# Performance work log

Measured on AMD Instinct MI355X. Metric: run time of the kernel, lower is better.

The kernel has to match this reference:

```python
import math
import jax, jax.numpy as jnp
import numpy as np

B, S, E = 8, 4096, 512


def setup_inputs() -> dict:
    key = jax.random.key(0)
    ks = jax.random.split(key, 8)
    w = 0.02
    return {
        "state1": jax.random.normal(ks[0], (B, S, E), jnp.float32),
        "state2": jax.random.normal(ks[1], (B, S, E), jnp.float32),
        "Wq": jax.random.normal(ks[2], (E, E), jnp.float32) * w,
        "bq": jax.random.normal(ks[3], (E,), jnp.float32) * w,
        "Wk": jax.random.normal(ks[4], (E, E), jnp.float32) * w,
        "bk": jax.random.normal(ks[5], (E,), jnp.float32) * w,
        "Wv": jax.random.normal(ks[6], (E, E), jnp.float32) * w,
        "bv": jax.random.normal(ks[7], (E,), jnp.float32) * w,
    }


def reference(state1, state2, Wq, bq, Wk, bk, Wv, bv):
    b, s, e = state1.shape
    num_blocks = max(1, int(math.ceil(s ** (2.0 / 3.0))))  # 256 for S=4096
    block_size = int(math.ceil(s / num_blocks))            # 16; exact tiling
    scale = math.sqrt(e)

    def proj(x, W, bias):  # torch Linear: x @ W.T + b
        return x @ W.T + bias

    # fold blocks into a batch dimension: [B, nb, bs, E]
    x1 = state1.reshape(b, num_blocks, block_size, e)
    x2 = state2.reshape(b, num_blocks, block_size, e)

    q1, k1, v1 = proj(x1, Wq, bq), proj(x1, Wk, bk), proj(x1, Wv, bv)
    q2, k2, v2 = proj(x2, Wq, bq), proj(x2, Wk, bk), proj(x2, Wv, bv)

    # block-diagonal bidirectional cross attention (dropout = eval/no-op)
    attn12 = jax.nn.softmax(jnp.einsum('bnqe,bnke->bnqk', q1, k2) / scale, axis=-1)
    out1 = jnp.einsum('bnqk,bnke->bnqe', attn12, v2).reshape(b, s, e)

    attn21 = jax.nn.softmax(jnp.einsum('bnqe,bnke->bnqk', q2, k1) / scale, axis=-1)
    out2 = jnp.einsum('bnqk,bnke->bnqe', attn21, v1).reshape(b, s, e)

    return out1, out2
```

## Files before the change

kernel.cpp:

```cpp
#include <hip/hip_runtime.h>
#include <hip/hip_bf16.h>

typedef __attribute__((ext_vector_type(4))) float f32x4;
typedef __attribute__((ext_vector_type(8))) short short8;
typedef __attribute__((ext_vector_type(4))) short short4v;

#define EDIM 512
#define WELEMS 262144

static __device__ __forceinline__ short f2bf(float f) {
  union { float f; unsigned u; } v; v.f = f;
  unsigned r = v.u + 0x7fffu + ((v.u >> 16) & 1u);
  return (short)(r >> 16);
}
static __device__ __forceinline__ float bf2f(short s) {
  union { float f; unsigned u; } v; v.u = ((unsigned)(unsigned short)s) << 16;
  return v.f;
}

static __device__ __forceinline__ void gload_lds16(const short* g, short* l) {
  __builtin_amdgcn_global_load_lds(
      (const __attribute__((address_space(1))) unsigned int*)g,
      (__attribute__((address_space(3))) unsigned int*)(unsigned int)(unsigned long long)l,
      16, 0, 0);
}

__global__ __launch_bounds__(256) void prep(
    const float* __restrict__ Wq, const float* __restrict__ bq,
    const float* __restrict__ Wk, const float* __restrict__ Wv,
    short* __restrict__ Wvb, float* __restrict__ tvec, short* __restrict__ Hb) {
  __shared__ float sh[2][64][33];
  const int b = blockIdx.x;
  const int tid = threadIdx.x;
  if (b < 256) {
    int i = (b * 256 + tid) * 4;
    f32x4 v = *(const f32x4*)(Wv + i);
    short4v vs;
#pragma unroll
    for (int j = 0; j < 4; ++j) vs[j] = f2bf(v[j]);
    *(short4v*)(Wvb + i) = vs;
  } else if (b < 264) {
    float* red = &sh[0][0][0];
    const int fl = tid & 63;
    const int part = tid >> 6;
    const int f = (b - 256) * 64 + fl;
    float s = 0.f;
    const int n0 = part * 128;
#pragma unroll 8
    for (int n = n0; n < n0 + 128; ++n) s += Wk[(size_t)n * EDIM + f] * bq[n];
    red[part * 64 + fl] = s;
    __syncthreads();
    if (part == 0)
      tvec[f] = ((red[fl] + red[64 + fl]) + (red[128 + fl] + red[192 + fl]));
  } else {
    const int hb = b - 264;
    const int bf = (hb >> 4) * 32;
    const int be = (hb & 15) * 32;
    const int fh = (tid & 15) * 2;
    const int eh = (tid >> 4) * 2;
    float a00 = 0, a01 = 0, a10 = 0, a11 = 0;
    for (int nc = 0; nc < 8; ++nc) {
      __syncthreads();
#pragma unroll
      for (int p = 0; p < 8; ++p) {
        const int idx = p * 256 + tid;
        const int n = idx >> 5, f = idx & 31;
        sh[0][n][f] = Wk[(size_t)(nc * 64 + n) * EDIM + bf + f];
        sh[1][n][f] = Wq[(size_t)(nc * 64 + n) * EDIM + be + f];
      }
      __syncthreads();
#pragma unroll 4
      for (int n = 0; n < 64; ++n) {
        const float k0 = sh[0][n][fh], k1 = sh[0][n][fh + 1];
        const float q0 = sh[1][n][eh], q1 = sh[1][n][eh + 1];
        a00 += k0 * q0; a01 += k0 * q1; a10 += k1 * q0; a11 += k1 * q1;
      }
    }
    Hb[(size_t)(bf + fh) * EDIM + be + eh] = f2bf(a00);
    Hb[(size_t)(bf + fh) * EDIM + be + eh + 1] = f2bf(a01);
    Hb[(size_t)(bf + fh + 1) * EDIM + be + eh] = f2bf(a10);
    Hb[(size_t)(bf + fh + 1) * EDIM + be + eh + 1] = f2bf(a11);
  }
}

__global__ __launch_bounds__(256) void convert_x(
    const float* __restrict__ s1, const float* __restrict__ s2,
    const float* __restrict__ tvec,
    short* __restrict__ o1, short* __restrict__ o2,
    float* __restrict__ w1, float* __restrict__ w2) {
  const int wv = threadIdx.x >> 6, lane = threadIdx.x & 63;
  const size_t r = (size_t)blockIdx.x * 4 + wv;
  const int off = lane * 8;
  const f32x4 t0 = *(const f32x4*)(tvec + off);
  const f32x4 t1 = *(const f32x4*)(tvec + off + 4);
#pragma unroll
  for (int st = 0; st < 2; ++st) {
    const float* src = st ? s2 : s1;
    f32x4 a0 = *(const f32x4*)(src + r * EDIM + off);
    f32x4 a1 = *(const f32x4*)(src + r * EDIM + off + 4);
    short8 rb;
    float dot = 0.f;
#pragma unroll
    for (int j = 0; j < 4; ++j) {
      rb[j] = f2bf(a0[j]); dot += a0[j] * t0[j];
      rb[j + 4] = f2bf(a1[j]); dot += a1[j] * t1[j];
    }
    *(short8*)((st ? o2 : o1) + r * EDIM + off) = rb;
#pragma unroll
    for (int d = 1; d < 64; d <<= 1) dot += __shfl_xor(dot, d);
    if (lane == 0) (st ? w2 : w1)[r] = dot;
  }
}

__global__ __launch_bounds__(256, 3) void proj_t(
    const short* __restrict__ S1b, const short* __restrict__ S2b,
    const short* __restrict__ Hb,
    short* __restrict__ TV, size_t McE, int mblocks) {
  __shared__ short Al[128 * 64];
  __shared__ short Bl[128 * 64];

  int mb, zn;
  {
    const int L = blockIdx.x;
    if ((mblocks & 7) == 0) {
      const int mpx = mblocks >> 3;
      const int xcd = L & 7;
      const int slot = L >> 3;
      mb = xcd * mpx + slot / 8;
      zn = slot % 8;
    } else { mb = L / 8; zn = L % 8; }
  }
  const int z = zn >> 2;
  const int nb = zn & 3;

  const short* __restrict__ X = z ? S2b : S1b;
  short* __restrict__ O = TV + (size_t)z * McE;

  const int m0 = mb * 128;
  const int n0 = nb * 128;
  const int tid = threadIdx.x;
  const int lane = tid & 63;
  const int wv = tid >> 6;
  const int wr = wv >> 1, wc = wv & 1;
  const int col = lane & 15;
  const int kg = lane >> 4;

  f32x4 acc[4][4] = {};

  for (int ks = 0; ks < EDIM / 64; ++ks) {
    const int k0 = ks * 64;
    __syncthreads();
#pragma unroll
    for (int j = 0; j < 4; ++j) {
      const int g = (j * 4 + wv) * 64 + lane;
      const int row = g >> 3;
      const int sc = (g & 7) ^ (row & 7);
      gload_lds16(X + (size_t)(m0 + row) * EDIM + k0 + sc * 8, Al + (j * 4 + wv) * 512);
      gload_lds16(Hb + (size_t)(n0 + row) * EDIM + k0 + sc * 8, Bl + (j * 4 + wv) * 512);
    }
    __syncthreads();
#pragma unroll
    for (int kk = 0; kk < 2; ++kk) {
      short8 af[4], bf8[4];
#pragma unroll
      for (int i = 0; i < 4; ++i) {
        const int ra = wr * 64 + i * 16 + col;
        const int rb = wc * 64 + i * 16 + col;
        af[i]  = *(const short8*)(Al + ra * 64 + ((((kk << 2) + kg) ^ (ra & 7)) << 3));
        bf8[i] = *(const short8*)(Bl + rb * 64 + ((((kk << 2) + kg) ^ (rb & 7)) << 3));
      }
#pragma unroll
      for (int mi = 0; mi < 4; ++mi)
#pragma unroll
        for (int nj = 0; nj < 4; ++nj)
          acc[mi][nj] = __builtin_amdgcn_mfma_f32_16x16x32_bf16(af[mi], bf8[nj], acc[mi][nj], 0, 0, 0);
    }
  }

#pragma unroll
  for (int mi = 0; mi < 4; ++mi) {
#pragma unroll
    for (int j = 0; j < 4; ++j) {
      const size_t r = m0 + wr * 64 + mi * 16 + kg * 4 + j;
#pragma unroll
      for (int nj = 0; nj < 4; ++nj) {
        const int e = n0 + wc * 64 + nj * 16 + col;
        O[r * EDIM + e] = f2bf(acc[mi][nj][j]);
      }
    }
  }
}

__global__ __launch_bounds__(256) void attn_y(
    const short* __restrict__ TV, const short* __restrict__ S1b, const short* __restrict__ S2b,
    const float* __restrict__ w1, const float* __restrict__ w2, size_t McE) {
  __shared__ float plds[4][16][16];
  const int dir = blockIdx.y;
  const short* __restrict__ Q = TV + (size_t)dir * McE;
  const short* __restrict__ KV = dir ? S1b : S2b;
  const float* __restrict__ w = dir ? w1 : w2;
  short* __restrict__ Y = (short*)TV + (size_t)(2 + dir) * McE;

  const int lane = threadIdx.x & 63;
  const int wv = threadIdx.x >> 6;
  const size_t r0 = ((size_t)blockIdx.x * 4 + wv) * 16;
  const int col = lane & 15;
  const int kg = lane >> 4;

  const short* Qp = Q + (r0 + col) * EDIM + kg * 8;
  const short* Kp = KV + (r0 + col) * EDIM + kg * 8;
  f32x4 s = {};
#pragma unroll
  for (int ks = 0; ks < 16; ++ks) {
    short8 a = *(const short8*)(Qp + ks * 32);
    short8 b = *(const short8*)(Kp + ks * 32);
    s = __builtin_amdgcn_mfma_f32_16x16x32_bf16(a, b, s, 0, 0, 0);
  }
  const float scale = 0.04419417382415922f;
  const float wj = w[r0 + col];
  float p[4];
#pragma unroll
  for (int j = 0; j < 4; ++j) p[j] = (s[j] + wj) * scale;
#pragma unroll
  for (int j = 0; j < 4; ++j) {
    float m = p[j];
#pragma unroll
    for (int d = 1; d < 16; d <<= 1) m = fmaxf(m, __shfl_xor(m, d));
    float e = __expf(p[j] - m);
    float ssum = e;
#pragma unroll
    for (int d = 1; d < 16; d <<= 1) ssum += __shfl_xor(ssum, d);
    p[j] = e / ssum;
  }
#pragma unroll
  for (int j = 0; j < 4; ++j) plds[wv][kg * 4 + j][col] = p[j];
  __syncthreads();

  const int e0 = lane * 8;
  short8 v8[16];
#pragma unroll
  for (int k = 0; k < 16; ++k) v8[k] = *(const short8*)(KV + (r0 + k) * EDIM + e0);
#pragma unroll
  for (int q = 0; q < 16; ++q) {
    float acc[8] = {0, 0, 0, 0, 0, 0, 0, 0};
#pragma unroll
    for (int k = 0; k < 16; ++k) {
      const float pv = plds[wv][q][k];
#pragma unroll
      for (int i = 0; i < 8; ++i) acc[i] += pv * bf2f(v8[k][i]);
    }
    short8 y;
#pragma unroll
    for (int i = 0; i < 8; ++i) y[i] = f2bf(acc[i]);
    *(short8*)(Y + (r0 + q) * EDIM + e0) = y;
  }
}

__global__ __launch_bounds__(256, 3) void out_gemm(
    const short* __restrict__ TV, const short* __restrict__ Wvb,
    const float* __restrict__ bv,
    float* __restrict__ out1, float* __restrict__ out2, size_t McE, int mblocks) {
  __shared__ short Al[128 * 64];
  __shared__ short Bl[128 * 64];

  int mb, zn;
  {
    const int L = blockIdx.x;
    if ((mblocks & 7) == 0) {
      const int mpx = mblocks >> 3;
      const int xcd = L & 7;
      const int slot = L >> 3;
      mb = xcd * mpx + slot / 8;
      zn = slot % 8;
    } else { mb = L / 8; zn = L % 8; }
  }
  const int z = zn >> 2;
  const int nb = zn & 3;

  const short* __restrict__ A = TV + (size_t)(2 + z) * McE;
  float* __restrict__ O = z ? out2 : out1;

  const int m0 = mb * 128;
  const int n0 = nb * 128;
  const int tid = threadIdx.x;
  const int lane = tid & 63;
  const int wv = tid >> 6;
  const int wr = wv >> 1, wc = wv & 1;
  const int col = lane & 15;
  const int kg = lane >> 4;

  f32x4 acc[4][4] = {};

  for (int ks = 0; ks < EDIM / 64; ++ks) {
    const int k0 = ks * 64;
    __syncthreads();
#pragma unroll
    for (int j = 0; j < 4; ++j) {
      const int g = (j * 4 + wv) * 64 + lane;
      const int row = g >> 3;
      const int sc = (g & 7) ^ (row & 7);
      gload_lds16(A + (size_t)(m0 + row) * EDIM + k0 + sc * 8, Al + (j * 4 + wv) * 512);
      gload_lds16(Wvb + (size_t)(n0 + row) * EDIM + k0 + sc * 8, Bl + (j * 4 + wv) * 512);
    }
    __syncthreads();
#pragma unroll
    for (int kk = 0; kk < 2; ++kk) {
      short8 af[4], bf8[4];
#pragma unroll
      for (int i = 0; i < 4; ++i) {
        const int ra = wr * 64 + i * 16 + col;
        const int rb = wc * 64 + i * 16 + col;
        af[i]  = *(const short8*)(Al + ra * 64 + ((((kk << 2) + kg) ^ (ra & 7)) << 3));
        bf8[i] = *(const short8*)(Bl + rb * 64 + ((((kk << 2) + kg) ^ (rb & 7)) << 3));
      }
#pragma unroll
      for (int mi = 0; mi < 4; ++mi)
#pragma unroll
        for (int nj = 0; nj < 4; ++nj)
          acc[mi][nj] = __builtin_amdgcn_mfma_f32_16x16x32_bf16(af[mi], bf8[nj], acc[mi][nj], 0, 0, 0);
    }
  }

#pragma unroll
  for (int mi = 0; mi < 4; ++mi) {
#pragma unroll
    for (int j = 0; j < 4; ++j) {
      const size_t r = m0 + wr * 64 + mi * 16 + kg * 4 + j;
#pragma unroll
      for (int nj = 0; nj < 4; ++nj) {
        const int e = n0 + wc * 64 + nj * 16 + col;
        O[r * EDIM + e] = acc[mi][nj][j] + bv[e];
      }
    }
  }
}

extern "C" void kernel_launch(void* const* d_in, const int* in_sizes, int n_in,
                              void* d_out, int out_size, void* d_ws, size_t ws_size,
                              hipStream_t stream) {
  const float* state1 = (const float*)d_in[0];
  const float* state2 = (const float*)d_in[1];
  const float* Wq = (const float*)d_in[2];
  const float* bq = (const float*)d_in[3];
  const float* Wk = (const float*)d_in[4];
  const float* Wv = (const float*)d_in[6];
  const float* bv = (const float*)d_in[7];

  const size_t Mtot = (size_t)8 * 4096;
  float* out1 = (float*)d_out;
  float* out2 = out1 + Mtot * EDIM;

  short* Wvb = (short*)d_ws;
  short* Hb = Wvb + WELEMS;
  float* tvec = (float*)(Hb + WELEMS);
  float* w1 = tvec + EDIM;
  float* w2 = w1 + Mtot;
  short* base = (short*)(w2 + Mtot);

  const size_t fixed_bytes = (size_t)(2 * WELEMS) * 2 + (EDIM + 2 * Mtot) * 4;
  size_t nch = 1;
  while (nch < 256) {
    size_t need = fixed_bytes + (size_t)6 * (Mtot / nch) * EDIM * 2;
    if (need <= ws_size) break;
    nch <<= 1;
  }
  const size_t Mc = Mtot / nch;
  const size_t McE = Mc * EDIM;
  const int mblocks = (int)(Mc / 128);
  short* S1b = base;
  short* S2b = S1b + McE;
  short* TV = S2b + McE;

  prep<<<dim3(520), dim3(256), 0, stream>>>(Wq, bq, Wk, Wv, Wvb, tvec, Hb);

  for (size_t c = 0; c < nch; ++c) {
    const size_t roff = c * Mc;
    convert_x<<<dim3((unsigned)(Mc / 4)), dim3(256), 0, stream>>>(
        state1 + roff * EDIM, state2 + roff * EDIM, tvec, S1b, S2b, w1 + roff, w2 + roff);
    proj_t<<<dim3((unsigned)(mblocks * 8)), dim3(256), 0, stream>>>(
        S1b, S2b, Hb, TV, McE, mblocks);
    attn_y<<<dim3((unsigned)(Mc / 64), 2), dim3(256), 0, stream>>>(
        TV, S1b, S2b, w1 + roff, w2 + roff, McE);
    out_gemm<<<dim3((unsigned)(mblocks * 8)), dim3(256), 0, stream>>>(
        TV, Wvb, bv, out1 + roff * EDIM, out2 + roff * EDIM, McE, mblocks);
  }
}
```

Before: 200.1 us.

## Merge weight prep into conversion kernel and compute key-bias term inside attention

The separate prep kernel is folded into the per-chunk conversion launch, so weight preprocessing runs as extra blocks of the first chunk's conversion grid. The per-row dot product of the keys with tvec moves out of the conversion kernel into attn_y, where it is computed from the bf16 keys already loaded for the score MFMA. This drops one launch and the w1/w2 workspace arrays. It adds ALU work in attn_y and now uses bf16-rounded keys for the bias term. The conversion blocks in the merged launch do not read tvec, so the new grid does not race on it.

```diff
diff --git a/kernel.cpp b/kernel.cpp
--- a/kernel.cpp
+++ b/kernel.cpp
@@ -25,90 +25,80 @@
       16, 0, 0);
 }
 
-__global__ __launch_bounds__(256) void prep(
+__global__ __launch_bounds__(256) void prep_convert(
+    const float* __restrict__ s1, const float* __restrict__ s2,
     const float* __restrict__ Wq, const float* __restrict__ bq,
     const float* __restrict__ Wk, const float* __restrict__ Wv,
-    short* __restrict__ Wvb, float* __restrict__ tvec, short* __restrict__ Hb) {
+    short* __restrict__ Wvb, float* __restrict__ tvec, short* __restrict__ Hb,
+    short* __restrict__ o1, short* __restrict__ o2, int prep_blocks) {
   __shared__ float sh[2][64][33];
   const int b = blockIdx.x;
   const int tid = threadIdx.x;
-  if (b < 256) {
-    int i = (b * 256 + tid) * 4;
-    f32x4 v = *(const f32x4*)(Wv + i);
-    short4v vs;
-#pragma unroll
-    for (int j = 0; j < 4; ++j) vs[j] = f2bf(v[j]);
-    *(short4v*)(Wvb + i) = vs;
-  } else if (b < 264) {
-    float* red = &sh[0][0][0];
-    const int fl = tid & 63;
-    const int part = tid >> 6;
-    const int f = (b - 256) * 64 + fl;
-    float s = 0.f;
-    const int n0 = part * 128;
+  if (b < prep_blocks) {
+    if (b < 256) {
+      int i = (b * 256 + tid) * 4;
+      f32x4 v = *(const f32x4*)(Wv + i);
+      short4v vs;
+#pragma unroll
+      for (int j = 0; j < 4; ++j) vs[j] = f2bf(v[j]);
+      *(short4v*)(Wvb + i) = vs;
+    } else if (b < 264) {
+      float* red = &sh[0][0][0];
+      const int fl = tid & 63;
+      const int part = tid >> 6;
+      const int f = (b - 256) * 64 + fl;
+      float s = 0.f;
+      const int n0 = part * 128;
 #pragma unroll 8
-    for (int n = n0; n < n0 + 128; ++n) s += Wk[(size_t)n * EDIM + f] * bq[n];
-    red[part * 64 + fl] = s;
-    __syncthreads();
-    if (part == 0)
-      tvec[f] = ((red[fl] + red[64 + fl]) + (red[128 + fl] + red[192 + fl]));
+      for (int n = n0; n < n0 + 128; ++n) s += Wk[(size_t)n * EDIM + f] * bq[n];
+      red[part * 64 + fl] = s;
+      __syncthreads();
+      if (part == 0)
+        tvec[f] = ((red[fl] + red[64 + fl]) + (red[128 + fl] + red[192 + fl]));
+    } else {
+      const int hb = b - 264;
+      const int bf = (hb >> 4) * 32;
+      const int be = (hb & 15) * 32;
+      const int fh = (tid & 15) * 2;
+      const int eh = (tid >> 4) * 2;
+      float a00 = 0, a01 = 0, a10 = 0, a11 = 0;
+      for (int nc = 0; nc < 8; ++nc) {
+        __syncthreads();
+#pragma unroll
+        for (int p = 0; p < 8; ++p) {
+          const int idx = p * 256 + tid;
+          const int n = idx >> 5, f = idx & 31;
+          sh[0][n][f] = Wk[(size_t)(nc * 64 + n) * EDIM + bf + f];
+          sh[1][n][f] = Wq[(size_t)(nc * 64 + n) * EDIM + be + f];
+        }
+        __syncthreads();
+#pragma unroll 4
+        for (int n = 0; n < 64; ++n) {
+          const float k0 = sh[0][n][fh], k1 = sh[0][n][fh + 1];
+          const float q0 = sh[1][n][eh], q1 = sh[1][n][eh + 1];
+          a00 += k0 * q0; a01 += k0 * q1; a10 += k1 * q0; a11 += k1 * q1;
+        }
+      }
+      Hb[(size_t)(bf + fh) * EDIM + be + eh] = f2bf(a00);
+      Hb[(size_t)(bf + fh) * EDIM + be + eh + 1] = f2bf(a01);
+      Hb[(size_t)(bf + fh + 1) * EDIM + be + eh] = f2bf(a10);
+      Hb[(size_t)(bf + fh + 1) * EDIM + be + eh + 1] = f2bf(a11);
+    }
   } else {
-    const int hb = b - 264;
-    const int bf = (hb >> 4) * 32;
-    const int be = (hb & 15) * 32;
-    const int fh = (tid & 15) * 2;
-    const int eh = (tid >> 4) * 2;
-    float a00 = 0, a01 = 0, a10 = 0, a11 = 0;
-    for (int nc = 0; nc < 8; ++nc) {
-      __syncthreads();
-#pragma unroll
-      for (int p = 0; p < 8; ++p) {
-        const int idx = p * 256 + tid;
-        const int n = idx >> 5, f = idx & 31;
-        sh[0][n][f] = Wk[(size_t)(nc * 64 + n) * EDIM + bf + f];
-        sh[1][n][f] = Wq[(size_t)(nc * 64 + n) * EDIM + be + f];
-      }
-      __syncthreads();
-#pragma unroll 4
-      for (int n = 0; n < 64; ++n) {
-        const float k0 = sh[0][n][fh], k1 = sh[0][n][fh + 1];
-        const float q0 = sh[1][n][eh], q1 = sh[1][n][eh + 1];
-        a00 += k0 * q0; a01 += k0 * q1; a10 += k1 * q0; a11 += k1 * q1;
-      }
-    }
-    Hb[(size_t)(bf + fh) * EDIM + be + eh] = f2bf(a00);
-    Hb[(size_t)(bf + fh) * EDIM + be + eh + 1] = f2bf(a01);
-    Hb[(size_t)(bf + fh + 1) * EDIM + be + eh] = f2bf(a10);
-    Hb[(size_t)(bf + fh + 1) * EDIM + be + eh + 1] = f2bf(a11);
-  }
-}
-
-__global__ __launch_bounds__(256) void convert_x(
-    const float* __restrict__ s1, const float* __restrict__ s2,
-    const float* __restrict__ tvec,
-    short* __restrict__ o1, short* __restrict__ o2,
-    float* __restrict__ w1, float* __restrict__ w2) {
-  const int wv = threadIdx.x >> 6, lane = threadIdx.x & 63;
-  const size_t r = (size_t)blockIdx.x * 4 + wv;
-  const int off = lane * 8;
-  const f32x4 t0 = *(const f32x4*)(tvec + off);
-  const f32x4 t1 = *(const f32x4*)(tvec + off + 4);
-#pragma unroll
-  for (int st = 0; st < 2; ++st) {
-    const float* src = st ? s2 : s1;
-    f32x4 a0 = *(const f32x4*)(src + r * EDIM + off);
-    f32x4 a1 = *(const f32x4*)(src + r * EDIM + off + 4);
-    short8 rb;
-    float dot = 0.f;
-#pragma unroll
-    for (int j = 0; j < 4; ++j) {
-      rb[j] = f2bf(a0[j]); dot += a0[j] * t0[j];
-      rb[j + 4] = f2bf(a1[j]); dot += a1[j] * t1[j];
-    }
-    *(short8*)((st ? o2 : o1) + r * EDIM + off) = rb;
-#pragma unroll
-    for (int d = 1; d < 64; d <<= 1) dot += __shfl_xor(dot, d);
-    if (lane == 0) (st ? w2 : w1)[r] = dot;
+    const int cb = b - prep_blocks;
+    const int wv = tid >> 6, lane = tid & 63;
+    const size_t r = (size_t)cb * 4 + wv;
+    const int off = lane * 8;
+#pragma unroll
+    for (int st = 0; st < 2; ++st) {
+      const float* src = st ? s2 : s1;
+      f32x4 a0 = *(const f32x4*)(src + r * EDIM + off);
+      f32x4 a1 = *(const f32x4*)(src + r * EDIM + off + 4);
+      short8 rb;
+#pragma unroll
+      for (int j = 0; j < 4; ++j) { rb[j] = f2bf(a0[j]); rb[j + 4] = f2bf(a1[j]); }
+      *(short8*)((st ? o2 : o1) + r * EDIM + off) = rb;
+    }
   }
 }
 
@@ -193,12 +183,11 @@
 
 __global__ __launch_bounds__(256) void attn_y(
     const short* __restrict__ TV, const short* __restrict__ S1b, const short* __restrict__ S2b,
-    const float* __restrict__ w1, const float* __restrict__ w2, size_t McE) {
+    const float* __restrict__ tvec, size_t McE) {
   __shared__ float plds[4][16][16];
   const int dir = blockIdx.y;
   const short* __restrict__ Q = TV + (size_t)dir * McE;
   const short* __restrict__ KV = dir ? S1b : S2b;
-  const float* __restrict__ w = dir ? w1 : w2;
   short* __restrict__ Y = (short*)TV + (size_t)(2 + dir) * McE;
 
   const int lane = threadIdx.x & 63;
@@ -210,17 +199,25 @@
   const short* Qp = Q + (r0 + col) * EDIM + kg * 8;
   const short* Kp = KV + (r0 + col) * EDIM + kg * 8;
   f32x4 s = {};
+  float wp = 0.f;
 #pragma unroll
   for (int ks = 0; ks < 16; ++ks) {
     short8 a = *(const short8*)(Qp + ks * 32);
     short8 b = *(const short8*)(Kp + ks * 32);
+    const f32x4 t0 = *(const f32x4*)(tvec + ks * 32 + kg * 8);
+    const f32x4 t1 = *(const f32x4*)(tvec + ks * 32 + kg * 8 + 4);
+#pragma unroll
+    for (int i = 0; i < 4; ++i)
+      wp += bf2f(b[i]) * t0[i] + bf2f(b[i + 4]) * t1[i];
     s = __builtin_amdgcn_mfma_f32_16x16x32_bf16(a, b, s, 0, 0, 0);
   }
+  wp += __shfl_xor(wp, 16);
+  wp += __shfl_xor(wp, 32);
+
   const float scale = 0.04419417382415922f;
-  const float wj = w[r0 + col];
   float p[4];
 #pragma unroll
-  for (int j = 0; j < 4; ++j) p[j] = (s[j] + wj) * scale;
+  for (int j = 0; j < 4; ++j) p[j] = (s[j] + wp) * scale;
 #pragma unroll
   for (int j = 0; j < 4; ++j) {
     float m = p[j];
@@ -353,11 +350,9 @@
   short* Wvb = (short*)d_ws;
   short* Hb = Wvb + WELEMS;
   float* tvec = (float*)(Hb + WELEMS);
-  float* w1 = tvec + EDIM;
-  float* w2 = w1 + Mtot;
-  short* base = (short*)(w2 + Mtot);
-
-  const size_t fixed_bytes = (size_t)(2 * WELEMS) * 2 + (EDIM + 2 * Mtot) * 4;
+  short* base = (short*)(tvec + EDIM);
+
+  const size_t fixed_bytes = (size_t)(2 * WELEMS) * 2 + EDIM * 4;
   size_t nch = 1;
   while (nch < 256) {
     size_t need = fixed_bytes + (size_t)6 * (Mtot / nch) * EDIM * 2;
@@ -371,16 +366,16 @@
   short* S2b = S1b + McE;
   short* TV = S2b + McE;
 
-  prep<<<dim3(520), dim3(256), 0, stream>>>(Wq, bq, Wk, Wv, Wvb, tvec, Hb);
-
   for (size_t c = 0; c < nch; ++c) {
     const size_t roff = c * Mc;
-    convert_x<<<dim3((unsigned)(Mc / 4)), dim3(256), 0, stream>>>(
-        state1 + roff * EDIM, state2 + roff * EDIM, tvec, S1b, S2b, w1 + roff, w2 + roff);
+    const int pb = (c == 0) ? 520 : 0;
+    prep_convert<<<dim3((unsigned)(Mc / 4 + pb)), dim3(256), 0, stream>>>(
+        state1 + roff * EDIM, state2 + roff * EDIM, Wq, bq, Wk, Wv,
+        Wvb, tvec, Hb, S1b, S2b, pb);
     proj_t<<<dim3((unsigned)(mblocks * 8)), dim3(256), 0, stream>>>(
         S1b, S2b, Hb, TV, McE, mblocks);
     attn_y<<<dim3((unsigned)(Mc / 64), 2), dim3(256), 0, stream>>>(
-        TV, S1b, S2b, w1 + roff, w2 + roff, McE);
+        TV, S1b, S2b, tvec, McE);
     out_gemm<<<dim3((unsigned)(mblocks * 8)), dim3(256), 0, stream>>>(
         TV, Wvb, bv, out1 + roff * EDIM, out2 + roff * EDIM, McE, mblocks);
   }
```

Result: faster. 183.9 us (-8.1%).
